# Kernel tuning notes

Hardware: AMD Instinct MI355X
Metric: run time of the kernel (lower is better)

## Reference

```python
import jax, jax.numpy as jnp
import numpy as np

INPUT_DIM = 1024
OUTPUT_DIM = 1024
DEGREE = 8


def setup_inputs() -> dict:
    key = jax.random.key(0)
    k1, k2 = jax.random.split(key)
    x = jax.random.normal(k1, (8192, INPUT_DIM), dtype=jnp.float32)
    std = 1.0 / (INPUT_DIM * (DEGREE + 1))
    cheby_coeffs = jax.random.normal(k2, (INPUT_DIM, OUTPUT_DIM, DEGREE + 1), dtype=jnp.float32) * std
    return {"x": x, "cheby_coeffs": cheby_coeffs}


def reference(x, cheby_coeffs):
    # x: [B, I]; cheby_coeffs: [I, O, D+1]
    degree = cheby_coeffs.shape[-1] - 1
    t = jnp.clip(jnp.tanh(x), -0.999, 0.999)            # [B, I]
    theta = jnp.arccos(t)[..., None]                     # [B, I, 1]
    arange = jnp.arange(degree + 1, dtype=x.dtype)       # [D+1]
    basis = jnp.cos(theta * arange)                      # [B, I, D+1] Chebyshev T_d(t)
    y = jnp.einsum('bid,iod->bo', basis, cheby_coeffs)   # [B, O]
    return y
```

## Files before the change

### kernel.cpp

```cpp
#include <hip/hip_runtime.h>
#include <stdint.h>

#define B_ROWS 8192
#define I_DIM  1024
#define N_DIM  1024
#define NDEG   9
#define K_DIM  (I_DIM * (NDEG-1))

typedef __attribute__((ext_vector_type(8)))  short short8;
typedef __attribute__((ext_vector_type(16))) float f32x16;

__device__ __forceinline__ unsigned short f2bf(float f) {
  union { float f; uint32_t u; } v; v.f = f;
  uint32_t u = v.u;
  u += 0x7FFFu + ((u >> 16) & 1u);
  return (unsigned short)(u >> 16);
}

__device__ __forceinline__ float bf2f(unsigned short h) {
  union { uint32_t u; float f; } v; v.u = ((uint32_t)h) << 16;
  return v.f;
}

__device__ __forceinline__ int rowhash(int r) {
  return (r & 7) ^ ((r >> 2) & 4);
}

__global__ __launch_bounds__(256) void basis_kernel(const float* __restrict__ x,
                                                    unsigned short* __restrict__ A) {
  const int b  = blockIdx.x;
  const int i0 = threadIdx.x * 4;
  const float4 xv = *reinterpret_cast<const float4*>(x + (size_t)b * I_DIM + i0);
  float t[4];
  t[0] = fminf(fmaxf(tanhf(xv.x), -0.999f), 0.999f);
  t[1] = fminf(fmaxf(tanhf(xv.y), -0.999f), 0.999f);
  t[2] = fminf(fmaxf(tanhf(xv.z), -0.999f), 0.999f);
  t[3] = fminf(fmaxf(tanhf(xv.w), -0.999f), 0.999f);

  unsigned short* outb = A + (size_t)b * K_DIM + i0;
  float Tp[4] = {1.f, 1.f, 1.f, 1.f};
  float Tc[4] = {t[0], t[1], t[2], t[3]};
  #pragma unroll
  for (int d = 1; d < NDEG; ++d) {
    ushort4 o4;
    o4.x = f2bf(Tc[0]); o4.y = f2bf(Tc[1]); o4.z = f2bf(Tc[2]); o4.w = f2bf(Tc[3]);
    *reinterpret_cast<ushort4*>(outb + (size_t)(d - 1) * I_DIM) = o4;
    if (d < NDEG - 1) {
      #pragma unroll
      for (int j = 0; j < 4; ++j) {
        float Tn = 2.0f * t[j] * Tc[j] - Tp[j];
        Tp[j] = Tc[j]; Tc[j] = Tn;
      }
    }
  }
}

__global__ __launch_bounds__(256) void repack_kernel(const float* __restrict__ cf,
                                                     unsigned short* __restrict__ Bt,
                                                     float* __restrict__ bias) {
  __shared__ unsigned short L[32][584];
  const int i0  = blockIdx.x * 32;
  const int o0  = blockIdx.y * 64;
  const int tid = threadIdx.x;

  #pragma unroll
  for (int j = 0; j < 18; ++j) {
    const int f4  = j * 256 + tid;
    const int il  = f4 / 144;
    const int odq = f4 % 144;
    const float4 v = *reinterpret_cast<const float4*>(
        cf + ((size_t)(i0 + il) * N_DIM + o0) * NDEG + (size_t)odq * 4);
    ushort4 w;
    w.x = f2bf(v.x); w.y = f2bf(v.y); w.z = f2bf(v.z); w.w = f2bf(v.w);
    *reinterpret_cast<ushort4*>(&L[il][odq * 4]) = w;
  }
  __syncthreads();

  for (int od = tid; od < 576; od += 256) {
    const int o = od / 9, d = od % 9;
    if (d == 0) {
      float s = 0.f;
      #pragma unroll
      for (int il = 0; il < 32; ++il) s += bf2f(L[il][od]);
      atomicAdd(&bias[o0 + o], s);
    } else {
      const size_t base = (size_t)(o0 + o) * K_DIM + (size_t)(d - 1) * I_DIM + i0;
      #pragma unroll
      for (int ci = 0; ci < 4; ++ci) {
        uint32_t uu[4];
        #pragma unroll
        for (int p = 0; p < 4; ++p) {
          unsigned short lo = L[ci * 8 + p * 2 + 0][od];
          unsigned short hi = L[ci * 8 + p * 2 + 1][od];
          uu[p] = (uint32_t)lo | ((uint32_t)hi << 16);
        }
        uint4 u; u.x = uu[0]; u.y = uu[1]; u.z = uu[2]; u.w = uu[3];
        *reinterpret_cast<uint4*>(Bt + base + ci * 8) = u;
      }
    }
  }
}

__global__ __launch_bounds__(256) void gemm_kernel(const unsigned short* __restrict__ A,
                                                   const unsigned short* __restrict__ Bt,
                                                   const float* __restrict__ bias,
                                                   float* __restrict__ C) {
  __shared__ unsigned short As[128 * 64];
  __shared__ unsigned short Bs[128 * 64];
  const int tid  = threadIdx.x;
  const int lane = tid & 63;
  const int wave = tid >> 6;
  const int l31  = lane & 31;
  const int half = lane >> 5;
  const int wm   = wave >> 1;
  const int wn   = wave & 1;
  const int m0   = blockIdx.x * 128;
  const int n0   = blockIdx.y * 128;

  const int sr   = tid >> 3;
  const int slot = tid & 7;

  f32x16 acc[2][2];
  #pragma unroll
  for (int a = 0; a < 2; ++a)
    #pragma unroll
    for (int b = 0; b < 2; ++b)
      #pragma unroll
      for (int r = 0; r < 16; ++r)
        acc[a][b][r] = 0.f;

  for (int kt = 0; kt < K_DIM / 64; ++kt) {
    const int k0 = kt * 64;
    #pragma unroll
    for (int s = 0; s < 4; ++s) {
      const int r  = s * 32 + sr;
      const int gc = slot ^ rowhash(r);
      const unsigned short* srcA = A + (size_t)(m0 + r) * K_DIM + k0 + gc * 8;
      __builtin_amdgcn_global_load_lds(
          (const __attribute__((address_space(1))) void*)srcA,
          (__attribute__((address_space(3))) void*)&As[r * 64 + slot * 8], 16, 0, 0);
      const unsigned short* srcB = Bt + (size_t)(n0 + r) * K_DIM + k0 + gc * 8;
      __builtin_amdgcn_global_load_lds(
          (const __attribute__((address_space(1))) void*)srcB,
          (__attribute__((address_space(3))) void*)&Bs[r * 64 + slot * 8], 16, 0, 0);
    }
    __syncthreads();

    short8 av[2][4], bv[2][4];
    #pragma unroll
    for (int mi = 0; mi < 2; ++mi) {
      const int row = wm * 64 + mi * 32 + l31;
      #pragma unroll
      for (int ks = 0; ks < 4; ++ks) {
        const int c  = ks * 2 + half;
        const int sl = c ^ rowhash(row);
        av[mi][ks] = *reinterpret_cast<const short8*>(&As[row * 64 + sl * 8]);
      }
    }
    #pragma unroll
    for (int ni = 0; ni < 2; ++ni) {
      const int row = wn * 64 + ni * 32 + l31;
      #pragma unroll
      for (int ks = 0; ks < 4; ++ks) {
        const int c  = ks * 2 + half;
        const int sl = c ^ rowhash(row);
        bv[ni][ks] = *reinterpret_cast<const short8*>(&Bs[row * 64 + sl * 8]);
      }
    }
    #pragma unroll
    for (int ks = 0; ks < 4; ++ks)
      #pragma unroll
      for (int mi = 0; mi < 2; ++mi)
        #pragma unroll
        for (int ni = 0; ni < 2; ++ni)
          acc[mi][ni] = __builtin_amdgcn_mfma_f32_32x32x16_bf16(av[mi][ks], bv[ni][ks],
                                                                acc[mi][ni], 0, 0, 0);
    __syncthreads();
  }

  #pragma unroll
  for (int ni = 0; ni < 2; ++ni) {
    const int col  = n0 + wn * 64 + ni * 32 + l31;
    const float bc = bias[col];
    #pragma unroll
    for (int mi = 0; mi < 2; ++mi) {
      const int rbase = m0 + wm * 64 + mi * 32 + 4 * half;
      #pragma unroll
      for (int r = 0; r < 16; ++r) {
        const int row = rbase + (r & 3) + 8 * (r >> 2);
        C[(size_t)row * N_DIM + col] = acc[mi][ni][r] + bc;
      }
    }
  }
}

extern "C" void kernel_launch(void* const* d_in, const int* in_sizes, int n_in,
                              void* d_out, int out_size, void* d_ws, size_t ws_size,
                              hipStream_t stream) {
  const float* x      = (const float*)d_in[0];
  const float* coeffs = (const float*)d_in[1];
  float* y            = (float*)d_out;

  const size_t bt_bytes = (size_t)N_DIM * K_DIM * sizeof(unsigned short);
  unsigned short* Bt = (unsigned short*)d_ws;
  float* bias        = (float*)((char*)d_ws + bt_bytes);
  unsigned short* A  = (unsigned short*)((char*)d_ws + bt_bytes + 4096);

  hipMemsetAsync(bias, 0, N_DIM * sizeof(float), stream);

  repack_kernel<<<dim3(I_DIM / 32, N_DIM / 64), 256, 0, stream>>>(coeffs, Bt, bias);

  size_t avail    = (ws_size > bt_bytes + 4096) ? (ws_size - bt_bytes - 4096) : 0;
  size_t rows_fit = avail / ((size_t)K_DIM * sizeof(unsigned short));
  int m_chunk = (int)((rows_fit / 128) * 128);
  if (m_chunk > B_ROWS) m_chunk = B_ROWS;
  if (m_chunk < 128)    m_chunk = 128;

  for (int m0 = 0; m0 < B_ROWS; m0 += m_chunk) {
    int mc = B_ROWS - m0; if (mc > m_chunk) mc = m_chunk;
    basis_kernel<<<mc, 256, 0, stream>>>(x + (size_t)m0 * I_DIM, A);
    gemm_kernel<<<dim3(mc / 128, N_DIM / 128), 256, 0, stream>>>(
        A, Bt, bias, y + (size_t)m0 * N_DIM);
  }
}
```

Measured before the change: 275.3 us.

## Fuse repack and basis prep, enlarge GEMM tile with double-buffered interleaved staging

The repack and basis kernels are merged into one prep launch so weight repacking and basis generation run concurrently and one launch is saved. The GEMM moves to a 256x128 tile with 512 threads (8 waves) and double-buffered LDS in 96KB of dynamic shared memory. Loads for the next k-tile are split into chunks and interleaved with MFMA phases, using explicit vmcnt waits, barriers and setprio to overlap global-to-LDS copies with compute. It also changes the LDS swizzle hash. The cost is more LDS per block and many barriers per k-step, and correctness depends on the hand-written wait counts.

```diff
diff --git a/kernel.cpp b/kernel.cpp
--- a/kernel.cpp
+++ b/kernel.cpp
@@ -7,6 +7,11 @@
 #define NDEG   9
 #define K_DIM  (I_DIM * (NDEG-1))
 
+#define BM 256
+#define BN 128
+#define BK 64
+#define NT (K_DIM / BK)
+
 typedef __attribute__((ext_vector_type(8)))  short short8;
 typedef __attribute__((ext_vector_type(16))) float f32x16;
 
@@ -22,91 +27,92 @@
   return v.f;
 }
 
-__device__ __forceinline__ int rowhash(int r) {
-  return (r & 7) ^ ((r >> 2) & 4);
-}
-
-__global__ __launch_bounds__(256) void basis_kernel(const float* __restrict__ x,
-                                                    unsigned short* __restrict__ A) {
-  const int b  = blockIdx.x;
-  const int i0 = threadIdx.x * 4;
-  const float4 xv = *reinterpret_cast<const float4*>(x + (size_t)b * I_DIM + i0);
-  float t[4];
-  t[0] = fminf(fmaxf(tanhf(xv.x), -0.999f), 0.999f);
-  t[1] = fminf(fmaxf(tanhf(xv.y), -0.999f), 0.999f);
-  t[2] = fminf(fmaxf(tanhf(xv.z), -0.999f), 0.999f);
-  t[3] = fminf(fmaxf(tanhf(xv.w), -0.999f), 0.999f);
-
-  unsigned short* outb = A + (size_t)b * K_DIM + i0;
-  float Tp[4] = {1.f, 1.f, 1.f, 1.f};
-  float Tc[4] = {t[0], t[1], t[2], t[3]};
-  #pragma unroll
-  for (int d = 1; d < NDEG; ++d) {
-    ushort4 o4;
-    o4.x = f2bf(Tc[0]); o4.y = f2bf(Tc[1]); o4.z = f2bf(Tc[2]); o4.w = f2bf(Tc[3]);
-    *reinterpret_cast<ushort4*>(outb + (size_t)(d - 1) * I_DIM) = o4;
-    if (d < NDEG - 1) {
-      #pragma unroll
-      for (int j = 0; j < 4; ++j) {
-        float Tn = 2.0f * t[j] * Tc[j] - Tp[j];
-        Tp[j] = Tc[j]; Tc[j] = Tn;
+__device__ __forceinline__ int h2(int r) { return (r >> 2) & 7; }
+
+__global__ __launch_bounds__(256) void prep_kernel(const float* __restrict__ x,
+                                                   const float* __restrict__ cf,
+                                                   unsigned short* __restrict__ A,
+                                                   unsigned short* __restrict__ Bt,
+                                                   float* __restrict__ bias,
+                                                   int repack_blocks) {
+  __shared__ unsigned short L[32][584];
+  const int tid = threadIdx.x;
+
+  if ((int)blockIdx.x < repack_blocks) {
+    const int bx = blockIdx.x;
+    const int i0 = (bx & 31) * 32;
+    const int o0 = (bx >> 5) * 64;
+
+    #pragma unroll
+    for (int j = 0; j < 18; ++j) {
+      const int f4  = j * 256 + tid;
+      const int il  = f4 / 144;
+      const int odq = f4 % 144;
+      const float4 v = *reinterpret_cast<const float4*>(
+          cf + ((size_t)(i0 + il) * N_DIM + o0) * NDEG + (size_t)odq * 4);
+      ushort4 w;
+      w.x = f2bf(v.x); w.y = f2bf(v.y); w.z = f2bf(v.z); w.w = f2bf(v.w);
+      *reinterpret_cast<ushort4*>(&L[il][odq * 4]) = w;
+    }
+    __syncthreads();
+
+    for (int od = tid; od < 576; od += 256) {
+      const int o = od / 9, d = od % 9;
+      if (d == 0) {
+        float s = 0.f;
+        #pragma unroll
+        for (int il = 0; il < 32; ++il) s += bf2f(L[il][od]);
+        atomicAdd(&bias[o0 + o], s);
+      } else {
+        const size_t base = (size_t)(o0 + o) * K_DIM + (size_t)(d - 1) * I_DIM + i0;
+        #pragma unroll
+        for (int ci = 0; ci < 4; ++ci) {
+          uint32_t uu[4];
+          #pragma unroll
+          for (int p = 0; p < 4; ++p) {
+            unsigned short lo = L[ci * 8 + p * 2 + 0][od];
+            unsigned short hi = L[ci * 8 + p * 2 + 1][od];
+            uu[p] = (uint32_t)lo | ((uint32_t)hi << 16);
+          }
+          uint4 u; u.x = uu[0]; u.y = uu[1]; u.z = uu[2]; u.w = uu[3];
+          *reinterpret_cast<uint4*>(Bt + base + ci * 8) = u;
+        }
       }
     }
-  }
-}
-
-__global__ __launch_bounds__(256) void repack_kernel(const float* __restrict__ cf,
-                                                     unsigned short* __restrict__ Bt,
-                                                     float* __restrict__ bias) {
-  __shared__ unsigned short L[32][584];
-  const int i0  = blockIdx.x * 32;
-  const int o0  = blockIdx.y * 64;
-  const int tid = threadIdx.x;
-
-  #pragma unroll
-  for (int j = 0; j < 18; ++j) {
-    const int f4  = j * 256 + tid;
-    const int il  = f4 / 144;
-    const int odq = f4 % 144;
-    const float4 v = *reinterpret_cast<const float4*>(
-        cf + ((size_t)(i0 + il) * N_DIM + o0) * NDEG + (size_t)odq * 4);
-    ushort4 w;
-    w.x = f2bf(v.x); w.y = f2bf(v.y); w.z = f2bf(v.z); w.w = f2bf(v.w);
-    *reinterpret_cast<ushort4*>(&L[il][odq * 4]) = w;
-  }
-  __syncthreads();
-
-  for (int od = tid; od < 576; od += 256) {
-    const int o = od / 9, d = od % 9;
-    if (d == 0) {
-      float s = 0.f;
-      #pragma unroll
-      for (int il = 0; il < 32; ++il) s += bf2f(L[il][od]);
-      atomicAdd(&bias[o0 + o], s);
-    } else {
-      const size_t base = (size_t)(o0 + o) * K_DIM + (size_t)(d - 1) * I_DIM + i0;
-      #pragma unroll
-      for (int ci = 0; ci < 4; ++ci) {
-        uint32_t uu[4];
+  } else {
+    const int b  = blockIdx.x - repack_blocks;
+    const int i0 = tid * 4;
+    const float4 xv = *reinterpret_cast<const float4*>(x + (size_t)b * I_DIM + i0);
+    float t[4];
+    t[0] = fminf(fmaxf(tanhf(xv.x), -0.999f), 0.999f);
+    t[1] = fminf(fmaxf(tanhf(xv.y), -0.999f), 0.999f);
+    t[2] = fminf(fmaxf(tanhf(xv.z), -0.999f), 0.999f);
+    t[3] = fminf(fmaxf(tanhf(xv.w), -0.999f), 0.999f);
+
+    unsigned short* outb = A + (size_t)b * K_DIM + i0;
+    float Tp[4] = {1.f, 1.f, 1.f, 1.f};
+    float Tc[4] = {t[0], t[1], t[2], t[3]};
+    #pragma unroll
+    for (int d = 1; d < NDEG; ++d) {
+      ushort4 o4;
+      o4.x = f2bf(Tc[0]); o4.y = f2bf(Tc[1]); o4.z = f2bf(Tc[2]); o4.w = f2bf(Tc[3]);
+      *reinterpret_cast<ushort4*>(outb + (size_t)(d - 1) * I_DIM) = o4;
+      if (d < NDEG - 1) {
         #pragma unroll
-        for (int p = 0; p < 4; ++p) {
-          unsigned short lo = L[ci * 8 + p * 2 + 0][od];
-          unsigned short hi = L[ci * 8 + p * 2 + 1][od];
-          uu[p] = (uint32_t)lo | ((uint32_t)hi << 16);
+        for (int j = 0; j < 4; ++j) {
+          float Tn = 2.0f * t[j] * Tc[j] - Tp[j];
+          Tp[j] = Tc[j]; Tc[j] = Tn;
         }
-        uint4 u; u.x = uu[0]; u.y = uu[1]; u.z = uu[2]; u.w = uu[3];
-        *reinterpret_cast<uint4*>(Bt + base + ci * 8) = u;
       }
     }
   }
 }
 
-__global__ __launch_bounds__(256) void gemm_kernel(const unsigned short* __restrict__ A,
-                                                   const unsigned short* __restrict__ Bt,
-                                                   const float* __restrict__ bias,
-                                                   float* __restrict__ C) {
-  __shared__ unsigned short As[128 * 64];
-  __shared__ unsigned short Bs[128 * 64];
+__global__ __launch_bounds__(512, 2) void gemm_kernel(const unsigned short* __restrict__ A,
+                                                      const unsigned short* __restrict__ Bt,
+                                                      const float* __restrict__ bias,
+                                                      float* __restrict__ C) {
+  extern __shared__ unsigned short sm[];
   const int tid  = threadIdx.x;
   const int lane = tid & 63;
   const int wave = tid >> 6;
@@ -114,11 +120,14 @@
   const int half = lane >> 5;
   const int wm   = wave >> 1;
   const int wn   = wave & 1;
-  const int m0   = blockIdx.x * 128;
-  const int n0   = blockIdx.y * 128;
+  const int m0   = blockIdx.x * BM;
+  const int n0   = blockIdx.y * BN;
 
   const int sr   = tid >> 3;
   const int slot = tid & 7;
+
+  const unsigned short* Abase = A  + (size_t)m0 * K_DIM;
+  const unsigned short* Bbase = Bt + (size_t)n0 * K_DIM;
 
   f32x16 acc[2][2];
   #pragma unroll
@@ -129,54 +138,84 @@
       for (int r = 0; r < 16; ++r)
         acc[a][b][r] = 0.f;
 
-  for (int kt = 0; kt < K_DIM / 64; ++kt) {
-    const int k0 = kt * 64;
-    #pragma unroll
-    for (int s = 0; s < 4; ++s) {
-      const int r  = s * 32 + sr;
-      const int gc = slot ^ rowhash(r);
-      const unsigned short* srcA = A + (size_t)(m0 + r) * K_DIM + k0 + gc * 8;
-      __builtin_amdgcn_global_load_lds(
-          (const __attribute__((address_space(1))) void*)srcA,
-          (__attribute__((address_space(3))) void*)&As[r * 64 + slot * 8], 16, 0, 0);
-      const unsigned short* srcB = Bt + (size_t)(n0 + r) * K_DIM + k0 + gc * 8;
-      __builtin_amdgcn_global_load_lds(
-          (const __attribute__((address_space(1))) void*)srcB,
-          (__attribute__((address_space(3))) void*)&Bs[r * 64 + slot * 8], 16, 0, 0);
-    }
-    __syncthreads();
-
-    short8 av[2][4], bv[2][4];
-    #pragma unroll
-    for (int mi = 0; mi < 2; ++mi) {
-      const int row = wm * 64 + mi * 32 + l31;
-      #pragma unroll
-      for (int ks = 0; ks < 4; ++ks) {
-        const int c  = ks * 2 + half;
-        const int sl = c ^ rowhash(row);
-        av[mi][ks] = *reinterpret_cast<const short8*>(&As[row * 64 + sl * 8]);
-      }
-    }
-    #pragma unroll
-    for (int ni = 0; ni < 2; ++ni) {
-      const int row = wn * 64 + ni * 32 + l31;
-      #pragma unroll
-      for (int ks = 0; ks < 4; ++ks) {
-        const int c  = ks * 2 + half;
-        const int sl = c ^ rowhash(row);
-        bv[ni][ks] = *reinterpret_cast<const short8*>(&Bs[row * 64 + sl * 8]);
-      }
-    }
+#define STAGE_A(s, bf, kk) { const int r_ = (s)*64 + sr; const int gc_ = slot ^ h2(r_);     \
+    __builtin_amdgcn_global_load_lds(                                                       \
+        (const __attribute__((address_space(1))) void*)(Abase + (size_t)r_*K_DIM + (kk) + gc_*8), \
+        (__attribute__((address_space(3))) void*)&sm[(bf)*16384 + r_*64 + slot*8], 16, 0, 0); }
+#define STAGE_B(s, bf, kk) { const int r_ = (s)*64 + sr; const int gc_ = slot ^ h2(r_);     \
+    __builtin_amdgcn_global_load_lds(                                                       \
+        (const __attribute__((address_space(1))) void*)(Bbase + (size_t)r_*K_DIM + (kk) + gc_*8), \
+        (__attribute__((address_space(3))) void*)&sm[32768 + (bf)*8192 + r_*64 + slot*8], 16, 0, 0); }
+
+  STAGE_A(0, 0, 0) STAGE_A(1, 0, 0) STAGE_A(2, 0, 0) STAGE_A(3, 0, 0)
+  STAGE_B(0, 0, 0) STAGE_B(1, 0, 0)
+
+  const int rowA0 = wm * 64 + l31;
+  const int rowA1 = wm * 64 + 32 + l31;
+  const int rowB0 = wn * 64 + l31;
+  const int rowB1 = wn * 64 + 32 + l31;
+
+  for (int kt = 0; kt < NT; ++kt) {
+    const int  cur  = kt & 1;
+    const int  nxt  = cur ^ 1;
+    const int  k1   = (kt + 1) * BK;
+    const bool more = (kt + 1 < NT);
+    const unsigned short* Asc = &sm[cur * 16384];
+    const unsigned short* Bsc = &sm[32768 + cur * 8192];
+
+    if (more) { STAGE_A(0, nxt, k1) STAGE_A(1, nxt, k1) }
+    if (more) asm volatile("s_waitcnt vmcnt(2)" ::: "memory");
+    else      asm volatile("s_waitcnt vmcnt(0)" ::: "memory");
+    __builtin_amdgcn_s_barrier();
+    __builtin_amdgcn_sched_barrier(0);
+
+    short8 av0[4], av1[4], bv0[4], bv1[4];
+    #pragma unroll
+    for (int ks = 0; ks < 4; ++ks) {
+      const int c = ks * 2 + half;
+      av0[ks] = *reinterpret_cast<const short8*>(&Asc[rowA0 * 64 + (c ^ h2(rowA0)) * 8]);
+      bv0[ks] = *reinterpret_cast<const short8*>(&Bsc[rowB0 * 64 + (c ^ h2(rowB0)) * 8]);
+    }
+    __builtin_amdgcn_s_setprio(1);
     #pragma unroll
     for (int ks = 0; ks < 4; ++ks)
-      #pragma unroll
-      for (int mi = 0; mi < 2; ++mi)
-        #pragma unroll
-        for (int ni = 0; ni < 2; ++ni)
-          acc[mi][ni] = __builtin_amdgcn_mfma_f32_32x32x16_bf16(av[mi][ks], bv[ni][ks],
-                                                                acc[mi][ni], 0, 0, 0);
-    __syncthreads();
-  }
+      acc[0][0] = __builtin_amdgcn_mfma_f32_32x32x16_bf16(av0[ks], bv0[ks], acc[0][0], 0, 0, 0);
+    __builtin_amdgcn_s_setprio(0);
+    __builtin_amdgcn_s_barrier();
+
+    #pragma unroll
+    for (int ks = 0; ks < 4; ++ks) {
+      const int c = ks * 2 + half;
+      bv1[ks] = *reinterpret_cast<const short8*>(&Bsc[rowB1 * 64 + (c ^ h2(rowB1)) * 8]);
+    }
+    if (more) { STAGE_A(2, nxt, k1) STAGE_A(3, nxt, k1) }
+    __builtin_amdgcn_s_barrier();
+    __builtin_amdgcn_s_setprio(1);
+    #pragma unroll
+    for (int ks = 0; ks < 4; ++ks)
+      acc[0][1] = __builtin_amdgcn_mfma_f32_32x32x16_bf16(av0[ks], bv1[ks], acc[0][1], 0, 0, 0);
+    __builtin_amdgcn_s_setprio(0);
+    __builtin_amdgcn_s_barrier();
+
+    #pragma unroll
+    for (int ks = 0; ks < 4; ++ks) {
+      const int c = ks * 2 + half;
+      av1[ks] = *reinterpret_cast<const short8*>(&Asc[rowA1 * 64 + (c ^ h2(rowA1)) * 8]);
+    }
+    if (more) { STAGE_B(0, nxt, k1) STAGE_B(1, nxt, k1) }
+    __builtin_amdgcn_s_barrier();
+    __builtin_amdgcn_s_setprio(1);
+    #pragma unroll
+    for (int ks = 0; ks < 4; ++ks) {
+      acc[1][0] = __builtin_amdgcn_mfma_f32_32x32x16_bf16(av1[ks], bv0[ks], acc[1][0], 0, 0, 0);
+      acc[1][1] = __builtin_amdgcn_mfma_f32_32x32x16_bf16(av1[ks], bv1[ks], acc[1][1], 0, 0, 0);
+    }
+    __builtin_amdgcn_s_setprio(0);
+    __builtin_amdgcn_s_barrier();
+    __builtin_amdgcn_sched_barrier(0);
+  }
+#undef STAGE_A
+#undef STAGE_B
 
   #pragma unroll
   for (int ni = 0; ni < 2; ++ni) {
@@ -208,18 +247,20 @@
 
   hipMemsetAsync(bias, 0, N_DIM * sizeof(float), stream);
 
-  repack_kernel<<<dim3(I_DIM / 32, N_DIM / 64), 256, 0, stream>>>(coeffs, Bt, bias);
+  hipFuncSetAttribute((const void*)gemm_kernel,
+                      hipFuncAttributeMaxDynamicSharedMemorySize, 98304);
 
   size_t avail    = (ws_size > bt_bytes + 4096) ? (ws_size - bt_bytes - 4096) : 0;
   size_t rows_fit = avail / ((size_t)K_DIM * sizeof(unsigned short));
-  int m_chunk = (int)((rows_fit / 128) * 128);
+  int m_chunk = (int)((rows_fit / BM) * BM);
   if (m_chunk > B_ROWS) m_chunk = B_ROWS;
-  if (m_chunk < 128)    m_chunk = 128;
+  if (m_chunk < BM)     m_chunk = BM;
 
   for (int m0 = 0; m0 < B_ROWS; m0 += m_chunk) {
     int mc = B_ROWS - m0; if (mc > m_chunk) mc = m_chunk;
-    basis_kernel<<<mc, 256, 0, stream>>>(x + (size_t)m0 * I_DIM, A);
-    gemm_kernel<<<dim3(mc / 128, N_DIM / 128), 256, 0, stream>>>(
+    const int rb = (m0 == 0) ? 512 : 0;
+    prep_kernel<<<rb + mc, 256, 0, stream>>>(x + (size_t)m0 * I_DIM, coeffs, A, Bt, bias, rb);
+    gemm_kernel<<<dim3(mc / BM, N_DIM / BN), 512, 98304, stream>>>(
         A, Bt, bias, y + (size_t)m0 * N_DIM);
   }
 }
```

Measured after the change: 274.6 us. Within noise of the previous version (-0.2%).
